# Optimization experiments

Measured on AMD Instinct MI355X. Metric: run time of the kernel, lower is better.

## Reference

```python
import jax, jax.numpy as jnp
import numpy as np

N_NODES = 100000
N_EDGES = 1600000
IN_C, HID_C, OUT_C = 128, 128, 40


def setup_inputs() -> dict:
    key = jax.random.key(0)
    ks = jax.random.split(key, 8)
    sd_in = 1.0 / np.sqrt(IN_C)
    sd_hid = 1.0 / np.sqrt(HID_C)
    return {
        "x": jax.random.normal(ks[0], (N_NODES, IN_C), dtype=jnp.float32),
        "edge_index": jax.random.randint(ks[1], (2, N_EDGES), 0, N_NODES, dtype=jnp.int64),
        # layer 1: lin_l (aggregated neighbors, with bias), lin_r (root, no bias)
        "W1l": jax.random.uniform(ks[2], (IN_C, HID_C), jnp.float32, -sd_in, sd_in),
        "W1r": jax.random.uniform(ks[3], (IN_C, HID_C), jnp.float32, -sd_in, sd_in),
        "b1": jnp.zeros((HID_C,), jnp.float32),
        # layer 2
        "W2l": jax.random.uniform(ks[4], (HID_C, OUT_C), jnp.float32, -sd_hid, sd_hid),
        "W2r": jax.random.uniform(ks[5], (HID_C, OUT_C), jnp.float32, -sd_hid, sd_hid),
        "b2": jnp.zeros((OUT_C,), jnp.float32),
    }


def _sage_conv(x, src, dst, Wl, Wr, b, num_nodes):
    # mean aggregation of source-node messages at destination nodes
    msg = x[src]                                          # [E, d] gather
    agg = jax.ops.segment_sum(msg, dst, num_segments=num_nodes)  # [N, d]
    cnt = jax.ops.segment_sum(jnp.ones((src.shape[0],), x.dtype), dst,
                              num_segments=num_nodes)     # [N]
    agg = agg / jnp.maximum(cnt, 1.0)[:, None]
    # lin_l(agg) + lin_r(x)  (bias lives in lin_l, matching PyG SAGEConv)
    return agg @ Wl + x @ Wr + b


def reference(x, edge_index, W1l, W1r, b1, W2l, W2r, b2):
    n = x.shape[0]
    src, dst = edge_index[0], edge_index[1]  # messages flow src -> dst
    h = jax.nn.relu(_sage_conv(x, src, dst, W1l, W1r, b1, n))
    # dropout p=0.0 -> identity
    out = _sage_conv(h, src, dst, W2l, W2r, b2, n)
    return jax.nn.log_softmax(out, axis=-1)
```

## Files before the change

### kernel.cpp

```cpp
#include <hip/hip_runtime.h>
#include <stdint.h>


typedef unsigned int uint32;
typedef unsigned short u16;
typedef __bf16 bf16x8 __attribute__((ext_vector_type(8)));
typedef float  f32x4  __attribute__((ext_vector_type(4)));
typedef unsigned short u16x8 __attribute__((ext_vector_type(8)));

#define CAPB 64
#define MAXE 2592
#define MAXN 104
#define RSST 112

__device__ __forceinline__ float bf2f(u16 u) {
    union { uint32 i; float f; } v; v.i = ((uint32)u) << 16; return v.f;
}
__device__ __forceinline__ u16 f2bf(float f) {
    union { float f; uint32 i; } v; v.f = f;
    uint32 i = v.i;
    uint32 r = (i + 0x7FFFu + ((i >> 16) & 1u)) >> 16;
    return (u16)r;
}

__global__ __launch_bounds__(256) void k_part1(const int* __restrict__ src,
        const int* __restrict__ dst, uint32* __restrict__ part,
        int* __restrict__ gcur, int E, int sw, uint32 magic, int cap) {
    __shared__ uint32 buf[1024];
    __shared__ int cnt8[8][8];
    __shared__ int base8[8][8];
    __shared__ int bstart[8], bn[8], gbase[8];
    int tid = threadIdx.x, rep = tid & 7;
    int ntiles = (E + 1023) >> 10;
    for (int tile = blockIdx.x; tile < ntiles; tile += gridDim.x) {
        if (tid < 64) cnt8[tid >> 3][tid & 7] = 0;
        __syncthreads();
        int e0 = (tile << 10) + tid * 4;
        int bk[4]; uint32 pk[4]; int nv = 0;
        if (e0 + 3 < E) {
            int4 d4 = *(const int4*)(dst + e0);
            int4 s4 = *(const int4*)(src + e0);
            int dd[4] = {d4.x, d4.y, d4.z, d4.w};
            int ss[4] = {s4.x, s4.y, s4.z, s4.w};
            nv = 4;
#pragma unroll
            for (int k = 0; k < 4; ++k) {
                bk[k] = (int)(((unsigned long long)(uint32)dd[k] * magic) >> 32);
                pk[k] = ((uint32)ss[k] << 14) | (uint32)(dd[k] - bk[k] * sw);
            }
        } else {
            for (int e = e0; e < E && e < e0 + 4; ++e) {
                int d = dst[e];
                int b = (int)(((unsigned long long)(uint32)d * magic) >> 32);
                bk[nv] = b;
                pk[nv] = ((uint32)src[e] << 14) | (uint32)(d - b * sw);
                ++nv;
            }
        }
        for (int k = 0; k < nv; ++k) atomicAdd(&cnt8[bk[k]][rep], 1);
        __syncthreads();
        if (tid == 0) {
            int run = 0;
            for (int b = 0; b < 8; ++b) {
                bstart[b] = run; int t0 = run;
                for (int r = 0; r < 8; ++r) { base8[b][r] = run; run += cnt8[b][r]; }
                bn[b] = run - t0;
            }
        }
        __syncthreads();
        if (tid < 64) cnt8[tid >> 3][tid & 7] = base8[tid >> 3][tid & 7];
        __syncthreads();
        for (int k = 0; k < nv; ++k) {
            int pos = atomicAdd(&cnt8[bk[k]][rep], 1);
            buf[pos] = pk[k];
        }
        if (tid < 8 && bn[tid] > 0)
            gbase[tid] = atomicAdd(&gcur[tid], bn[tid]);
        __syncthreads();
#pragma unroll
        for (int b = 0; b < 8; ++b) {
            int n = bn[b];
            if (n == 0) continue;
            int gb = gbase[b], bs = bstart[b];
            int lim = (b + 1) * cap;
            for (int i = tid; i < n; i += 256) {
                int p = gb + i;
                if (p < lim) part[p] = buf[bs + i];
            }
        }
        __syncthreads();
    }
}

__global__ __launch_bounds__(256) void k_part2(const uint32* __restrict__ part1,
        const int* __restrict__ gcur1, uint32* __restrict__ part2,
        int* __restrict__ gcur2, int cap1, int cap2, int sw2, uint32 magic2) {
    __shared__ uint32 buf[128][CAPB];
    __shared__ int lcnt[128], gbase[128];
    int s = blockIdx.x & 7;
    int m = gcur1[s] - s * cap1;
    const uint32* p1 = part1 + (size_t)s * cap1;
    int sbase = s * 128;
    int ntiles = (m + 2047) >> 11;
    for (int tile = blockIdx.x >> 3; tile < ntiles; tile += (gridDim.x >> 3)) {
        for (int i = threadIdx.x; i < 128; i += 256) lcnt[i] = 0;
        __syncthreads();
#pragma unroll
        for (int half = 0; half < 2; ++half) {
            int t0 = (tile << 11) + half * 1024 + threadIdx.x * 4;
            if (t0 + 3 < m) {
                uint4 v4 = *(const uint4*)(p1 + t0);
                uint32 vv[4] = {v4.x, v4.y, v4.z, v4.w};
#pragma unroll
                for (int k = 0; k < 4; ++k) {
                    uint32 dl = vv[k] & 16383u;
                    int sub = (int)(((unsigned long long)dl * magic2) >> 32);
                    uint32 pk = ((vv[k] >> 14) << 7) | (dl - (uint32)(sub * sw2));
                    int slot = atomicAdd(&lcnt[sub], 1);
                    if (slot < CAPB) buf[sub][slot] = pk;
                    else {
                        int p = atomicAdd(&gcur2[sbase + sub], 1);
                        if (p < (sbase + sub + 1) * cap2) part2[p] = pk;
                    }
                }
            } else {
                for (int idx = t0; idx < m && idx < t0 + 4; ++idx) {
                    uint32 v = p1[idx];
                    uint32 dl = v & 16383u;
                    int sub = (int)(((unsigned long long)dl * magic2) >> 32);
                    uint32 pk = ((v >> 14) << 7) | (dl - (uint32)(sub * sw2));
                    int slot = atomicAdd(&lcnt[sub], 1);
                    if (slot < CAPB) buf[sub][slot] = pk;
                    else {
                        int p = atomicAdd(&gcur2[sbase + sub], 1);
                        if (p < (sbase + sub + 1) * cap2) part2[p] = pk;
                    }
                }
            }
        }
        __syncthreads();
        if (threadIdx.x < 128) {
            int n = min(lcnt[threadIdx.x], CAPB);
            lcnt[threadIdx.x] = n;
            if (n > 0) gbase[threadIdx.x] = atomicAdd(&gcur2[sbase + threadIdx.x], n);
        }
        __syncthreads();
        int b = threadIdx.x >> 1, halfsel = threadIdx.x & 1;
        int n = lcnt[b];
        if (n > 0) {
            int gb = gbase[b];
            int lim = (sbase + b + 1) * cap2;
            for (int i = halfsel; i < n; i += 2) {
                int p = gb + i;
                if (p < lim) part2[p] = buf[b][i];
            }
        }
        __syncthreads();
    }
}

__global__ void k_prep(const float* __restrict__ W1l, const float* __restrict__ W1r,
                       const float* __restrict__ W2l, const float* __restrict__ W2r,
                       u16* __restrict__ Wt1, u16* __restrict__ Wt2,
                       int* __restrict__ gcur1, int cap1,
                       int* __restrict__ gcur2, int cap2) {
    if (blockIdx.x == 0 && threadIdx.x < 8) gcur1[threadIdx.x] = threadIdx.x * cap1;
    if (blockIdx.x < 4) {
        int idx = blockIdx.x * 256 + threadIdx.x;
        gcur2[idx] = idx * cap2;
    }
    if (blockIdx.x < 128) {
        int idx = blockIdx.x * 256 + threadIdx.x;
        int c = idx >> 7, k = idx & 127;
        float v = (c < 128) ? W1l[k * 128 + c] : W1r[k * 128 + (c - 128)];
        Wt1[idx] = f2bf(v);
    } else {
        int idx = (blockIdx.x - 128) * 256 + threadIdx.x;
        int c = idx >> 7, k = idx & 127;
        const float* W = (c < 48) ? W2l : W2r;
        int cc = (c < 48) ? c : c - 48;
        float v = (cc < 40) ? W[k * 40 + cc] : 0.f;
        Wt2[idx] = f2bf(v);
    }
}

__global__ __launch_bounds__(512) void k_gemm1(const float* __restrict__ x,
        const u16* __restrict__ Wt,
        u16* __restrict__ z1, u16* __restrict__ r1, int N) {
    __shared__ u16 xs[128][136];
    int tid = threadIdx.x;
    int rbase = blockIdx.x * 128;
#pragma unroll
    for (int i = 0; i < 8; ++i) {
        int fi = tid + i * 512;
        int row = fi >> 5, c4 = fi & 31;
        int grow = rbase + row;
        grow = grow < N ? grow : N - 1;
        float4 v = *(const float4*)(x + ((size_t)grow << 7) + c4 * 4);
        ushort4 w4;
        w4.x = f2bf(v.x); w4.y = f2bf(v.y); w4.z = f2bf(v.z); w4.w = f2bf(v.w);
        *(ushort4*)&xs[row][c4 * 4] = w4;
    }

    int lane = tid & 63;
    int w    = tid >> 6;
    int l15 = lane & 15, g = lane >> 4;
    int rloc = (w >> 2) * 64;
    int cbase = (w & 3) * 64;

    bf16x8 Bf[4][4];
#pragma unroll
    for (int c = 0; c < 4; ++c)
#pragma unroll
        for (int ks = 0; ks < 4; ++ks)
            Bf[c][ks] = *(const bf16x8*)(Wt + (((size_t)(cbase + c * 16 + l15)) << 7)
                                            + ks * 32 + g * 8);

    f32x4 acc[4][4];
    f32x4 z4 = {0.f, 0.f, 0.f, 0.f};
#pragma unroll
    for (int r = 0; r < 4; ++r)
#pragma unroll
        for (int c = 0; c < 4; ++c) acc[r][c] = z4;

    __syncthreads();

#pragma unroll
    for (int ks = 0; ks < 4; ++ks) {
        bf16x8 Af[4];
#pragma unroll
        for (int r = 0; r < 4; ++r)
            Af[r] = *(const bf16x8*)&xs[rloc + r * 16 + l15][ks * 32 + g * 8];
#pragma unroll
        for (int r = 0; r < 4; ++r)
#pragma unroll
            for (int c = 0; c < 4; ++c)
                acc[r][c] = __builtin_amdgcn_mfma_f32_16x16x32_bf16(
                                Af[r], Bf[c][ks], acc[r][c], 0, 0, 0);
    }

#pragma unroll
    for (int r = 0; r < 4; ++r) {
#pragma unroll
        for (int c = 0; c < 4; ++c) {
            int col = cbase + c * 16 + l15;
            u16* out = (col < 128) ? z1 : r1;
            int cc = col & 127;
#pragma unroll
            for (int j = 0; j < 4; ++j) {
                int row = rbase + rloc + r * 16 + g * 4 + j;
                if (row < N) out[((size_t)row << 7) + cc] = f2bf(acc[r][c][j]);
            }
        }
    }
}

__global__ __launch_bounds__(256) void k_gemm2(const u16* __restrict__ hb,
        const u16* __restrict__ Wt2,
        u16* __restrict__ z2p, u16* __restrict__ r2, int N) {
    __shared__ u16 hs[128][136];
    int tid = threadIdx.x;
    int rbase = blockIdx.x * 128;
#pragma unroll
    for (int i = 0; i < 8; ++i) {
        int ci = tid + i * 256;
        int row = ci >> 4, c8 = ci & 15;
        int grow = rbase + row;
        grow = grow < N ? grow : N - 1;
        u16x8 v = *(const u16x8*)(hb + ((size_t)grow << 7) + c8 * 8);
        *(u16x8*)&hs[row][c8 * 8] = v;
    }

    int lane = tid & 63;
    int w    = tid >> 6;
    int l15 = lane & 15, g = lane >> 4;
    int rloc = (w >> 1) * 64;
    int half = w & 1;

    bf16x8 Bf[3][4];
#pragma unroll
    for (int c = 0; c < 3; ++c)
#pragma unroll
        for (int ks = 0; ks < 4; ++ks)
            Bf[c][ks] = *(const bf16x8*)(Wt2 + (((size_t)(half * 48 + c * 16 + l15)) << 7)
                                             + ks * 32 + g * 8);

    f32x4 acc[4][3];
    f32x4 z4 = {0.f, 0.f, 0.f, 0.f};
#pragma unroll
    for (int r = 0; r < 4; ++r)
#pragma unroll
        for (int c = 0; c < 3; ++c) acc[r][c] = z4;

    __syncthreads();

#pragma unroll
    for (int ks = 0; ks < 4; ++ks) {
        bf16x8 Af[4];
#pragma unroll
        for (int r = 0; r < 4; ++r)
            Af[r] = *(const bf16x8*)&hs[rloc + r * 16 + l15][ks * 32 + g * 8];
#pragma unroll
        for (int r = 0; r < 4; ++r)
#pragma unroll
            for (int c = 0; c < 3; ++c)
                acc[r][c] = __builtin_amdgcn_mfma_f32_16x16x32_bf16(
                                Af[r], Bf[c][ks], acc[r][c], 0, 0, 0);
    }

    if (half == 0) {
#pragma unroll
        for (int r = 0; r < 4; ++r)
#pragma unroll
            for (int c = 0; c < 3; ++c) {
                int col = c * 16 + l15;
#pragma unroll
                for (int j = 0; j < 4; ++j) {
                    int row = rbase + rloc + r * 16 + g * 4 + j;
                    if (row < N) z2p[((size_t)row << 6) + col] = f2bf(acc[r][c][j]);
                }
            }
        int row = rbase + rloc + lane;
        if (row < N) {
            u16x8 z8 = {0, 0, 0, 0, 0, 0, 0, 0};
            *(u16x8*)(z2p + ((size_t)row << 6) + 48) = z8;
            *(u16x8*)(z2p + ((size_t)row << 6) + 56) = z8;
        }
    } else {
#pragma unroll
        for (int r = 0; r < 4; ++r)
#pragma unroll
            for (int c = 0; c < 3; ++c) {
                int col = c * 16 + l15;
                if (col < 40) {
#pragma unroll
                    for (int j = 0; j < 4; ++j) {
                        int row = rbase + rloc + r * 16 + g * 4 + j;
                        if (row < N) r2[(size_t)row * 40 + col] = f2bf(acc[r][c][j]);
                    }
                }
            }
    }
}

__global__ __launch_bounds__(512) void k_agg1_f(const u16* __restrict__ z1,
        const u16* __restrict__ r1, const float* __restrict__ b1,
        uint32* __restrict__ part2, const int* __restrict__ gcur2,
        u16* __restrict__ h, int* __restrict__ rsg,
        int N, int sw1, int sw2, int cap2) {
    __shared__ uint32 ebuf[MAXE];
    __shared__ uint32 esrt[MAXE];
    __shared__ int cnt[MAXN], cur[MAXN], rs[MAXN + 32];
    int b = blockIdx.x, s = b >> 7, sub = b & 127;
    int nb = s * sw1 + sub * sw2;
    int slice_end = min((s + 1) * sw1, N);
    int nn = min(sw2, slice_end - nb);
    if (nn <= 0) return;
    int tid = threadIdx.x;
    int m2 = gcur2[b] - b * cap2;
    m2 = min(m2, min(cap2, MAXE));
    uint32* p2 = part2 + (size_t)b * cap2;

    for (int i = tid; i < m2; i += 512) ebuf[i] = p2[i];
    for (int i = tid; i < nn; i += 512) cnt[i] = 0;
    __syncthreads();
    for (int i = tid; i < m2; i += 512) atomicAdd(&cnt[ebuf[i] & 127], 1);
    __syncthreads();
    if (tid < 64) {
        int c0 = (tid < nn) ? cnt[tid] : 0;
        int c1 = (64 + tid < nn) ? cnt[64 + tid] : 0;
        for (int off = 1; off < 64; off <<= 1) {
            int t0 = __shfl_up(c0, off, 64);
            int t1 = __shfl_up(c1, off, 64);
            if (tid >= off) { c0 += t0; c1 += t1; }
        }
        int tot0 = __shfl(c0, 63, 64);
        if (tid == 0) rs[0] = 0;
        rs[tid + 1] = c0;
        rs[64 + tid + 1] = tot0 + c1;
    }
    __syncthreads();
    for (int i = tid; i < nn; i += 512) cur[i] = rs[i];
    __syncthreads();
    for (int i = tid; i < m2; i += 512) {
        uint32 v = ebuf[i];
        int pos = atomicAdd(&cur[v & 127], 1);
        esrt[pos] = v >> 7;
    }
    __syncthreads();

    for (int i = tid; i < m2; i += 512) p2[i] = esrt[i];
    for (int i = tid; i <= nn; i += 512) rsg[b * RSST + i] = rs[i];

    int lane = tid & 63, wv = tid >> 6;
    int g = lane >> 4, c = lane & 15;
    for (int node = wv; node < nn; node += 8) {
        int s0 = rs[node], s1 = rs[node + 1];
        float acc[8];
#pragma unroll
        for (int i = 0; i < 8; ++i) acc[i] = 0.f;
        int j = s0 + g;
        for (; j + 12 < s1; j += 16) {
            int sA = esrt[j], sB = esrt[j + 4];
            int sC = esrt[j + 8], sD = esrt[j + 12];
            u16x8 a = *(const u16x8*)(z1 + ((size_t)sA << 7) + c * 8);
            u16x8 bb = *(const u16x8*)(z1 + ((size_t)sB << 7) + c * 8);
            u16x8 d = *(const u16x8*)(z1 + ((size_t)sC << 7) + c * 8);
            u16x8 e = *(const u16x8*)(z1 + ((size_t)sD << 7) + c * 8);
#pragma unroll
            for (int i = 0; i < 8; ++i)
                acc[i] += (bf2f(a[i]) + bf2f(bb[i])) + (bf2f(d[i]) + bf2f(e[i]));
        }
        for (; j + 4 < s1; j += 8) {
            int sA = esrt[j], sB = esrt[j + 4];
            u16x8 a = *(const u16x8*)(z1 + ((size_t)sA << 7) + c * 8);
            u16x8 bb = *(const u16x8*)(z1 + ((size_t)sB << 7) + c * 8);
#pragma unroll
            for (int i = 0; i < 8; ++i) acc[i] += bf2f(a[i]) + bf2f(bb[i]);
        }
        if (j < s1) {
            int sA = esrt[j];
            u16x8 a = *(const u16x8*)(z1 + ((size_t)sA << 7) + c * 8);
#pragma unroll
            for (int i = 0; i < 8; ++i) acc[i] += bf2f(a[i]);
        }
#pragma unroll
        for (int i = 0; i < 8; ++i) {
            acc[i] += __shfl_xor(acc[i], 16, 64);
            acc[i] += __shfl_xor(acc[i], 32, 64);
        }
        if (g == 0) {
            float inv = 1.0f / fmaxf((float)(s1 - s0), 1.0f);
            size_t go = ((size_t)(nb + node) << 7) + c * 8;
            u16x8 rv = *(const u16x8*)(r1 + go);
            float4 b0 = *(const float4*)(b1 + c * 8);
            float4 b4 = *(const float4*)(b1 + c * 8 + 4);
            float bbv[8] = {b0.x, b0.y, b0.z, b0.w, b4.x, b4.y, b4.z, b4.w};
            u16x8 o;
#pragma unroll
            for (int i = 0; i < 8; ++i)
                o[i] = f2bf(fmaxf(acc[i] * inv + bf2f(rv[i]) + bbv[i], 0.f));
            *(u16x8*)(h + go) = o;
        }
    }
}

__global__ __launch_bounds__(512) void k_agg2_f(const u16* __restrict__ z2p,
        const u16* __restrict__ r2, const float* __restrict__ b2,
        const uint32* __restrict__ part2, const int* __restrict__ gcur2,
        const int* __restrict__ rsg, float* __restrict__ out,
        int N, int sw1, int sw2, int cap2) {
    __shared__ uint32 esrt[MAXE];
    __shared__ int rs[MAXN + 1];
    int b = blockIdx.x, s = b >> 7, sub = b & 127;
    int nb = s * sw1 + sub * sw2;
    int slice_end = min((s + 1) * sw1, N);
    int nn = min(sw2, slice_end - nb);
    if (nn <= 0) return;
    int tid = threadIdx.x;
    int m2 = gcur2[b] - b * cap2;
    m2 = min(m2, min(cap2, MAXE));
    const uint32* p2 = part2 + (size_t)b * cap2;

    for (int i = tid; i < m2; i += 512) esrt[i] = p2[i];
    for (int i = tid; i <= nn; i += 512) rs[i] = rsg[b * RSST + i];
    __syncthreads();

    int lane = tid & 63, wv = tid >> 6;
    int le = lane >> 3, c = lane & 7;
    bool act = c < 5;
    for (int node = wv; node < nn; node += 8) {
        int s0 = rs[node], s1 = rs[node + 1];
        float acc[8];
#pragma unroll
        for (int i = 0; i < 8; ++i) acc[i] = 0.f;
        int j = s0 + le;
        for (; j + 8 < s1; j += 16) {
            int sA = esrt[j], sB = esrt[j + 8];
            u16x8 a = *(const u16x8*)(z2p + ((size_t)sA << 6) + c * 8);
            u16x8 bb = *(const u16x8*)(z2p + ((size_t)sB << 6) + c * 8);
#pragma unroll
            for (int i = 0; i < 8; ++i) acc[i] += bf2f(a[i]) + bf2f(bb[i]);
        }
        if (j < s1) {
            int sA = esrt[j];
            u16x8 a = *(const u16x8*)(z2p + ((size_t)sA << 6) + c * 8);
#pragma unroll
            for (int i = 0; i < 8; ++i) acc[i] += bf2f(a[i]);
        }
#pragma unroll
        for (int i = 0; i < 8; ++i) {
            acc[i] += __shfl_xor(acc[i], 8, 64);
            acc[i] += __shfl_xor(acc[i], 16, 64);
            acc[i] += __shfl_xor(acc[i], 32, 64);
        }
        if (le == 0) {
            float inv = 1.0f / fmaxf((float)(s1 - s0), 1.0f);
            float v[8];
            if (act) {
                u16x8 rv = *(const u16x8*)(r2 + (size_t)(nb + node) * 40 + c * 8);
                float4 b0 = *(const float4*)(b2 + c * 8);
                float4 b4 = *(const float4*)(b2 + c * 8 + 4);
                float bbv[8] = {b0.x, b0.y, b0.z, b0.w, b4.x, b4.y, b4.z, b4.w};
#pragma unroll
                for (int i = 0; i < 8; ++i) v[i] = acc[i] * inv + bf2f(rv[i]) + bbv[i];
            } else {
#pragma unroll
                for (int i = 0; i < 8; ++i) v[i] = -1e30f;
            }
            float m = v[0];
#pragma unroll
            for (int i = 1; i < 8; ++i) m = fmaxf(m, v[i]);
            m = fmaxf(m, __shfl_xor(m, 1, 64));
            m = fmaxf(m, __shfl_xor(m, 2, 64));
            m = fmaxf(m, __shfl_xor(m, 4, 64));
            float sum = 0.f;
            if (act) {
#pragma unroll
                for (int i = 0; i < 8; ++i) sum += __expf(v[i] - m);
            }
            sum += __shfl_xor(sum, 1, 64);
            sum += __shfl_xor(sum, 2, 64);
            sum += __shfl_xor(sum, 4, 64);
            float lse = __logf(sum);
            if (act) {
                float4 o0, o4;
                o0.x = v[0] - m - lse; o0.y = v[1] - m - lse;
                o0.z = v[2] - m - lse; o0.w = v[3] - m - lse;
                o4.x = v[4] - m - lse; o4.y = v[5] - m - lse;
                o4.z = v[6] - m - lse; o4.w = v[7] - m - lse;
                *(float4*)(out + (size_t)(nb + node) * 40 + c * 8) = o0;
                *(float4*)(out + (size_t)(nb + node) * 40 + c * 8 + 4) = o4;
            }
        }
    }
}

extern "C" void kernel_launch(void* const* d_in, const int* in_sizes, int n_in,
                              void* d_out, int out_size, void* d_ws, size_t ws_size,
                              hipStream_t stream) {
    const float* x   = (const float*)d_in[0];
    const int*   ei  = (const int*)d_in[1];
    const float* W1l = (const float*)d_in[2];
    const float* W1r = (const float*)d_in[3];
    const float* b1  = (const float*)d_in[4];
    const float* W2l = (const float*)d_in[5];
    const float* W2r = (const float*)d_in[6];
    const float* b2  = (const float*)d_in[7];
    float* out = (float*)d_out;

    int N = in_sizes[0] / 128;
    int E = in_sizes[1] / 2;
    const int* esrc = ei;
    const int* edst = ei + E;

    int sw1 = (N + 7) / 8;
    int sw2 = (sw1 + 127) / 128;
    uint32 magic1 = (uint32)((((unsigned long long)1 << 32) + sw1 - 1) / sw1);
    uint32 magic2 = (uint32)((((unsigned long long)1 << 32) + sw2 - 1) / sw2);
    int cap1 = (((E >> 3) + 8192) + 3) & ~3;
    int cap2 = (((E >> 10) + 1024) + 3) & ~3;

    char* p = (char*)d_ws;
    size_t off = 0;
    auto alloc = [&](size_t bytes) {
        void* q = p + off;
        off = (off + bytes + 255) & ~(size_t)255;
        return q;
    };
    int* gcur1 = (int*)alloc(64);
    int* gcur2 = (int*)alloc(1024 * 4);
    int* rsg   = (int*)alloc((size_t)1024 * RSST * 4);
    u16* Wt1 = (u16*)alloc(256 * 128 * 2);
    u16* Wt2 = (u16*)alloc(96 * 128 * 2);
    uint32* part1 = (uint32*)alloc((size_t)8 * cap1 * 4);
    uint32* part2 = (uint32*)alloc((size_t)1024 * cap2 * 4);
    u16* z1 = (u16*)alloc((size_t)N * 128 * 2);
    u16* r1 = (u16*)alloc((size_t)N * 128 * 2);
    u16* hb = r1;
    u16* z2p = z1;
    u16* r2  = z1 + (size_t)N * 64;

    k_prep<<<176, 256, 0, stream>>>(W1l, W1r, W2l, W2r, Wt1, Wt2,
                                    gcur1, cap1, gcur2, cap2);
    k_part1<<<1024, 256, 0, stream>>>(esrc, edst, part1, gcur1, E, sw1, magic1, cap1);
    k_part2<<<784, 256, 0, stream>>>(part1, gcur1, part2, gcur2, cap1, cap2,
                                     sw2, magic2);

    k_gemm1<<<(N + 127) / 128, 512, 0, stream>>>(x, Wt1, z1, r1, N);
    k_agg1_f<<<1024, 512, 0, stream>>>(z1, r1, b1, part2, gcur2, hb, rsg,
                                       N, sw1, sw2, cap2);
    k_gemm2<<<(N + 127) / 128, 256, 0, stream>>>(hb, Wt2, z2p, r2, N);
    k_agg2_f<<<1024, 512, 0, stream>>>(z2p, r2, b2, part2, gcur2, rsg, out,
                                       N, sw1, sw2, cap2);
}
```

Baseline: 199.0 us.

## Merge edge partition pass and layer-1 GEMM into one heterogeneous launch

Folds the first edge-bucketing pass and the layer-1 GEMM into a single kernel whose blocks take either a 2048-edge partition tile or a 128-row GEMM tile, chosen by block index. The two independent stages can then run concurrently on the GPU, and one launch plus one serialization point go away. The second partition pass now handles 4096 edges per tile with a larger per-bucket shared buffer (CAPB 96) and half as many blocks. In exchange, the partition blocks now run at 512 threads with one tile each, and the larger shared-memory footprint may lower occupancy.

```diff
diff --git a/kernel.cpp b/kernel.cpp
--- a/kernel.cpp
+++ b/kernel.cpp
@@ -8,7 +8,7 @@
 typedef float  f32x4  __attribute__((ext_vector_type(4)));
 typedef unsigned short u16x8 __attribute__((ext_vector_type(8)));
 
-#define CAPB 64
+#define CAPB 96
 #define MAXE 2592
 #define MAXN 104
 #define RSST 112
@@ -23,19 +23,48 @@
     return (u16)r;
 }
 
-__global__ __launch_bounds__(256) void k_part1(const int* __restrict__ src,
-        const int* __restrict__ dst, uint32* __restrict__ part,
-        int* __restrict__ gcur, int E, int sw, uint32 magic, int cap) {
-    __shared__ uint32 buf[1024];
-    __shared__ int cnt8[8][8];
-    __shared__ int base8[8][8];
-    __shared__ int bstart[8], bn[8], gbase[8];
-    int tid = threadIdx.x, rep = tid & 7;
-    int ntiles = (E + 1023) >> 10;
-    for (int tile = blockIdx.x; tile < ntiles; tile += gridDim.x) {
+__global__ void k_prep(const float* __restrict__ W1l, const float* __restrict__ W1r,
+                       const float* __restrict__ W2l, const float* __restrict__ W2r,
+                       u16* __restrict__ Wt1, u16* __restrict__ Wt2,
+                       int* __restrict__ gcur1, int cap1,
+                       int* __restrict__ gcur2, int cap2) {
+    if (blockIdx.x == 0 && threadIdx.x < 8) gcur1[threadIdx.x] = threadIdx.x * cap1;
+    if (blockIdx.x < 4) {
+        int idx = blockIdx.x * 256 + threadIdx.x;
+        gcur2[idx] = idx * cap2;
+    }
+    if (blockIdx.x < 128) {
+        int idx = blockIdx.x * 256 + threadIdx.x;
+        int c = idx >> 7, k = idx & 127;
+        float v = (c < 128) ? W1l[k * 128 + c] : W1r[k * 128 + (c - 128)];
+        Wt1[idx] = f2bf(v);
+    } else {
+        int idx = (blockIdx.x - 128) * 256 + threadIdx.x;
+        int c = idx >> 7, k = idx & 127;
+        const float* W = (c < 48) ? W2l : W2r;
+        int cc = (c < 48) ? c : c - 48;
+        float v = (cc < 40) ? W[k * 40 + cc] : 0.f;
+        Wt2[idx] = f2bf(v);
+    }
+}
+
+__global__ __launch_bounds__(512) void k_fused1(
+        const int* __restrict__ src, const int* __restrict__ dst,
+        uint32* __restrict__ part, int* __restrict__ gcur,
+        int E, int sw, uint32 magic, int cap, int nt1,
+        const float* __restrict__ x, const u16* __restrict__ Wt,
+        u16* __restrict__ z1, u16* __restrict__ r1, int N) {
+    int tid = threadIdx.x;
+    if ((int)blockIdx.x < nt1) {
+        __shared__ uint32 buf[2048];
+        __shared__ int cnt8[8][8];
+        __shared__ int base8[8][8];
+        __shared__ int bstart[8], bn[8], gbase[8];
+        int rep = tid & 7;
+        int tile = blockIdx.x;
         if (tid < 64) cnt8[tid >> 3][tid & 7] = 0;
         __syncthreads();
-        int e0 = (tile << 10) + tid * 4;
+        int e0 = (tile << 11) + tid * 4;
         int bk[4]; uint32 pk[4]; int nv = 0;
         if (e0 + 3 < E) {
             int4 d4 = *(const int4*)(dst + e0);
@@ -83,12 +112,77 @@
             if (n == 0) continue;
             int gb = gbase[b], bs = bstart[b];
             int lim = (b + 1) * cap;
-            for (int i = tid; i < n; i += 256) {
+            for (int i = tid; i < n; i += 512) {
                 int p = gb + i;
                 if (p < lim) part[p] = buf[bs + i];
             }
         }
-        __syncthreads();
+    } else {
+        __shared__ u16 xs[128][136];
+        int rbase = ((int)blockIdx.x - nt1) * 128;
+#pragma unroll
+        for (int i = 0; i < 8; ++i) {
+            int fi = tid + i * 512;
+            int row = fi >> 5, c4 = fi & 31;
+            int grow = rbase + row;
+            grow = grow < N ? grow : N - 1;
+            float4 v = *(const float4*)(x + ((size_t)grow << 7) + c4 * 4);
+            ushort4 w4;
+            w4.x = f2bf(v.x); w4.y = f2bf(v.y); w4.z = f2bf(v.z); w4.w = f2bf(v.w);
+            *(ushort4*)&xs[row][c4 * 4] = w4;
+        }
+
+        int lane = tid & 63;
+        int w    = tid >> 6;
+        int l15 = lane & 15, g = lane >> 4;
+        int rloc = (w >> 2) * 64;
+        int cbase = (w & 3) * 64;
+
+        bf16x8 Bf[4][4];
+#pragma unroll
+        for (int c = 0; c < 4; ++c)
+#pragma unroll
+            for (int ks = 0; ks < 4; ++ks)
+                Bf[c][ks] = *(const bf16x8*)(Wt + (((size_t)(cbase + c * 16 + l15)) << 7)
+                                                + ks * 32 + g * 8);
+
+        f32x4 acc[4][4];
+        f32x4 z4 = {0.f, 0.f, 0.f, 0.f};
+#pragma unroll
+        for (int r = 0; r < 4; ++r)
+#pragma unroll
+            for (int c = 0; c < 4; ++c) acc[r][c] = z4;
+
+        __syncthreads();
+
+#pragma unroll
+        for (int ks = 0; ks < 4; ++ks) {
+            bf16x8 Af[4];
+#pragma unroll
+            for (int r = 0; r < 4; ++r)
+                Af[r] = *(const bf16x8*)&xs[rloc + r * 16 + l15][ks * 32 + g * 8];
+#pragma unroll
+            for (int r = 0; r < 4; ++r)
+#pragma unroll
+                for (int c = 0; c < 4; ++c)
+                    acc[r][c] = __builtin_amdgcn_mfma_f32_16x16x32_bf16(
+                                    Af[r], Bf[c][ks], acc[r][c], 0, 0, 0);
+        }
+
+#pragma unroll
+        for (int r = 0; r < 4; ++r) {
+#pragma unroll
+            for (int c = 0; c < 4; ++c) {
+                int col = cbase + c * 16 + l15;
+                u16* out = (col < 128) ? z1 : r1;
+                int cc = col & 127;
+#pragma unroll
+                for (int j = 0; j < 4; ++j) {
+                    int row = rbase + rloc + r * 16 + g * 4 + j;
+                    if (row < N) out[((size_t)row << 7) + cc] = f2bf(acc[r][c][j]);
+                }
+            }
+        }
     }
 }
 
@@ -101,13 +195,13 @@
     int m = gcur1[s] - s * cap1;
     const uint32* p1 = part1 + (size_t)s * cap1;
     int sbase = s * 128;
-    int ntiles = (m + 2047) >> 11;
+    int ntiles = (m + 4095) >> 12;
     for (int tile = blockIdx.x >> 3; tile < ntiles; tile += (gridDim.x >> 3)) {
         for (int i = threadIdx.x; i < 128; i += 256) lcnt[i] = 0;
         __syncthreads();
 #pragma unroll
-        for (int half = 0; half < 2; ++half) {
-            int t0 = (tile << 11) + half * 1024 + threadIdx.x * 4;
+        for (int q = 0; q < 4; ++q) {
+            int t0 = (tile << 12) + q * 1024 + threadIdx.x * 4;
             if (t0 + 3 < m) {
                 uint4 v4 = *(const uint4*)(p1 + t0);
                 uint32 vv[4] = {v4.x, v4.y, v4.z, v4.w};
@@ -159,102 +253,6 @@
     }
 }
 
-__global__ void k_prep(const float* __restrict__ W1l, const float* __restrict__ W1r,
-                       const float* __restrict__ W2l, const float* __restrict__ W2r,
-                       u16* __restrict__ Wt1, u16* __restrict__ Wt2,
-                       int* __restrict__ gcur1, int cap1,
-                       int* __restrict__ gcur2, int cap2) {
-    if (blockIdx.x == 0 && threadIdx.x < 8) gcur1[threadIdx.x] = threadIdx.x * cap1;
-    if (blockIdx.x < 4) {
-        int idx = blockIdx.x * 256 + threadIdx.x;
-        gcur2[idx] = idx * cap2;
-    }
-    if (blockIdx.x < 128) {
-        int idx = blockIdx.x * 256 + threadIdx.x;
-        int c = idx >> 7, k = idx & 127;
-        float v = (c < 128) ? W1l[k * 128 + c] : W1r[k * 128 + (c - 128)];
-        Wt1[idx] = f2bf(v);
-    } else {
-        int idx = (blockIdx.x - 128) * 256 + threadIdx.x;
-        int c = idx >> 7, k = idx & 127;
-        const float* W = (c < 48) ? W2l : W2r;
-        int cc = (c < 48) ? c : c - 48;
-        float v = (cc < 40) ? W[k * 40 + cc] : 0.f;
-        Wt2[idx] = f2bf(v);
-    }
-}
-
-__global__ __launch_bounds__(512) void k_gemm1(const float* __restrict__ x,
-        const u16* __restrict__ Wt,
-        u16* __restrict__ z1, u16* __restrict__ r1, int N) {
-    __shared__ u16 xs[128][136];
-    int tid = threadIdx.x;
-    int rbase = blockIdx.x * 128;
-#pragma unroll
-    for (int i = 0; i < 8; ++i) {
-        int fi = tid + i * 512;
-        int row = fi >> 5, c4 = fi & 31;
-        int grow = rbase + row;
-        grow = grow < N ? grow : N - 1;
-        float4 v = *(const float4*)(x + ((size_t)grow << 7) + c4 * 4);
-        ushort4 w4;
-        w4.x = f2bf(v.x); w4.y = f2bf(v.y); w4.z = f2bf(v.z); w4.w = f2bf(v.w);
-        *(ushort4*)&xs[row][c4 * 4] = w4;
-    }
-
-    int lane = tid & 63;
-    int w    = tid >> 6;
-    int l15 = lane & 15, g = lane >> 4;
-    int rloc = (w >> 2) * 64;
-    int cbase = (w & 3) * 64;
-
-    bf16x8 Bf[4][4];
-#pragma unroll
-    for (int c = 0; c < 4; ++c)
-#pragma unroll
-        for (int ks = 0; ks < 4; ++ks)
-            Bf[c][ks] = *(const bf16x8*)(Wt + (((size_t)(cbase + c * 16 + l15)) << 7)
-                                            + ks * 32 + g * 8);
-
-    f32x4 acc[4][4];
-    f32x4 z4 = {0.f, 0.f, 0.f, 0.f};
-#pragma unroll
-    for (int r = 0; r < 4; ++r)
-#pragma unroll
-        for (int c = 0; c < 4; ++c) acc[r][c] = z4;
-
-    __syncthreads();
-
-#pragma unroll
-    for (int ks = 0; ks < 4; ++ks) {
-        bf16x8 Af[4];
-#pragma unroll
-        for (int r = 0; r < 4; ++r)
-            Af[r] = *(const bf16x8*)&xs[rloc + r * 16 + l15][ks * 32 + g * 8];
-#pragma unroll
-        for (int r = 0; r < 4; ++r)
-#pragma unroll
-            for (int c = 0; c < 4; ++c)
-                acc[r][c] = __builtin_amdgcn_mfma_f32_16x16x32_bf16(
-                                Af[r], Bf[c][ks], acc[r][c], 0, 0, 0);
-    }
-
-#pragma unroll
-    for (int r = 0; r < 4; ++r) {
-#pragma unroll
-        for (int c = 0; c < 4; ++c) {
-            int col = cbase + c * 16 + l15;
-            u16* out = (col < 128) ? z1 : r1;
-            int cc = col & 127;
-#pragma unroll
-            for (int j = 0; j < 4; ++j) {
-                int row = rbase + rloc + r * 16 + g * 4 + j;
-                if (row < N) out[((size_t)row << 7) + cc] = f2bf(acc[r][c][j]);
-            }
-        }
-    }
-}
-
 __global__ __launch_bounds__(256) void k_gemm2(const u16* __restrict__ hb,
         const u16* __restrict__ Wt2,
         u16* __restrict__ z2p, u16* __restrict__ r2, int N) {
@@ -581,13 +579,16 @@
     u16* z2p = z1;
     u16* r2  = z1 + (size_t)N * 64;
 
+    int nt1 = (E + 2047) >> 11;
+    int ng1 = (N + 127) / 128;
+
     k_prep<<<176, 256, 0, stream>>>(W1l, W1r, W2l, W2r, Wt1, Wt2,
                                     gcur1, cap1, gcur2, cap2);
-    k_part1<<<1024, 256, 0, stream>>>(esrc, edst, part1, gcur1, E, sw1, magic1, cap1);
-    k_part2<<<784, 256, 0, stream>>>(part1, gcur1, part2, gcur2, cap1, cap2,
+    k_fused1<<<nt1 + ng1, 512, 0, stream>>>(esrc, edst, part1, gcur1,
+                                            E, sw1, magic1, cap1, nt1,
+                                            x, Wt1, z1, r1, N);
+    k_part2<<<392, 256, 0, stream>>>(part1, gcur1, part2, gcur2, cap1, cap2,
                                      sw2, magic2);
-
-    k_gemm1<<<(N + 127) / 128, 512, 0, stream>>>(x, Wt1, z1, r1, N);
     k_agg1_f<<<1024, 512, 0, stream>>>(z1, r1, b1, part2, gcur2, hb, rsg,
                                        N, sw1, sw2, cap2);
     k_gemm2<<<(N + 127) / 128, 256, 0, stream>>>(hb, Wt2, z2p, r2, N);
```

New measurement: 183.4 us (median of 2 runs). 1.08x faster.
